# Kernel tuning notes

Hardware: AMD Instinct MI355X
Metric: run time of the kernel (lower is better)

Reference implementation:

```python
import jax, jax.numpy as jnp
import numpy as np

NUM_LAYERS = 4
EMBED = 1024
HEADS = 16
QKV = 1024
MLP = 4096
EPS_LN = 1e-6


def _layernorm(x, scale, bias):
    m = jnp.mean(x, axis=-1, keepdims=True)
    v = jnp.mean(jnp.square(x - m), axis=-1, keepdims=True)
    return (x - m) * jax.lax.rsqrt(v + EPS_LN) * scale + bias


def setup_inputs() -> dict:
    key = jax.random.key(0)
    ks = jax.random.split(key, 12)
    B, L = 4, 1024
    s = 0.02
    inp = {
        "queries": jax.random.normal(ks[0], (B, L, EMBED), dtype=jnp.float32),
        "Wq": jax.random.normal(ks[1], (NUM_LAYERS, EMBED, QKV), dtype=jnp.float32) * s,
        "bq": jnp.zeros((NUM_LAYERS, QKV), dtype=jnp.float32),
        "Wk": jax.random.normal(ks[2], (NUM_LAYERS, EMBED, QKV), dtype=jnp.float32) * s,
        "bk": jnp.zeros((NUM_LAYERS, QKV), dtype=jnp.float32),
        "Wv": jax.random.normal(ks[3], (NUM_LAYERS, EMBED, QKV), dtype=jnp.float32) * s,
        "bv": jnp.zeros((NUM_LAYERS, QKV), dtype=jnp.float32),
        "Wo": jax.random.normal(ks[4], (NUM_LAYERS, QKV, EMBED), dtype=jnp.float32) * s,
        "bo": jnp.zeros((NUM_LAYERS, EMBED), dtype=jnp.float32),
        "ln1_s": jnp.ones((NUM_LAYERS, EMBED), dtype=jnp.float32),
        "ln1_b": jnp.zeros((NUM_LAYERS, EMBED), dtype=jnp.float32),
        "ln2_s": jnp.ones((NUM_LAYERS, EMBED), dtype=jnp.float32),
        "ln2_b": jnp.zeros((NUM_LAYERS, EMBED), dtype=jnp.float32),
        "W1": jax.random.normal(ks[5], (NUM_LAYERS, EMBED, MLP), dtype=jnp.float32) * s,
        "b1": jnp.zeros((NUM_LAYERS, MLP), dtype=jnp.float32),
        "W2": jax.random.normal(ks[6], (NUM_LAYERS, MLP, EMBED), dtype=jnp.float32) * s,
        "b2": jnp.zeros((NUM_LAYERS, EMBED), dtype=jnp.float32),
    }
    return inp


def _block(x, Wq, bq, Wk, bk, Wv, bv, Wo, bo, ln1_s, ln1_b, ln2_s, ln2_b, W1, b1, W2, b2):
    # post-norm block (pre_norm=False)
    B, L, _ = x.shape
    head_dim = EMBED // HEADS
    q = (x @ Wq + bq).reshape(B, L, HEADS, head_dim)
    k = (x @ Wk + bk).reshape(B, L, HEADS, head_dim)
    v = (x @ Wv + bv).reshape(B, L, HEADS, head_dim)
    q = q / (head_dim ** 0.5)
    attn = jnp.einsum("bqhd,bkhd->bhqk", q, k)
    attn = jax.nn.softmax(attn, axis=-1)
    upd = jnp.einsum("bhqk,bkhd->bqhd", attn, v)  # [B,L,H,hd]
    a = upd.reshape(B, L, QKV) @ Wo + bo
    h = _layernorm(a + x, ln1_s, ln1_b)
    z = jax.nn.relu(h @ W1 + b1) @ W2 + b2
    return _layernorm(z + h, ln2_s, ln2_b)


def reference(queries, Wq, bq, Wk, bk, Wv, bv, Wo, bo, ln1_s, ln1_b, ln2_s, ln2_b, W1, b1, W2, b2):
    x = queries
    for l in range(NUM_LAYERS):
        x = _block(x, Wq[l], bq[l], Wk[l], bk[l], Wv[l], bv[l], Wo[l], bo[l],
                   ln1_s[l], ln1_b[l], ln2_s[l], ln2_b[l], W1[l], b1[l], W2[l], b2[l])
    return x
```

## Files before the change

kernel.cpp:

```cpp
#include <hip/hip_runtime.h>
#include <stdint.h>

typedef __bf16 bf16;
typedef __bf16 bf16x8 __attribute__((ext_vector_type(8)));
typedef float floatx4 __attribute__((ext_vector_type(4)));

#define LOG2E 1.44269504088896340736f

__device__ __forceinline__ void gl2lds16(const bf16* g, bf16* l) {
    __builtin_amdgcn_global_load_lds((__attribute__((address_space(1))) void*)g,
                                     (__attribute__((address_space(3))) void*)l,
                                     16, 0, 0);
}

template<int COLS>
__device__ __forceinline__ int swz(int ch, int r) {
    if constexpr (COLS == 32) return ch ^ ((r >> 1) & 3);
    else                      return ch ^ (r & 7);
}

template<int ROWS, int COLS>
__device__ __forceinline__ void stage_tile_sw(bf16* lds, const bf16* g, int srcStride, int wave, int lane) {
    constexpr int NINST = (ROWS * COLS * 2) / 1024;
    constexpr int ROWB  = COLS * 2;
    #pragma unroll
    for (int u = 0; u < NINST / 4; ++u) {
        int t  = wave + u * 4;
        int ob = t * 1024 + lane * 16;
        int r  = ob / ROWB;
        int ch = (ob % ROWB) >> 4;
        int sc = swz<COLS>(ch, r);
        gl2lds16(g + r * srcStride + sc * 8, lds + t * 512);
    }
}

template<int RELU, int OUTF, int OUTB>
__device__ __forceinline__ void gemm_core(const bf16* __restrict__ A, const bf16* __restrict__ Bt,
                                          const float* __restrict__ bias, float scale,
                                          float* __restrict__ outf, bf16* __restrict__ outb,
                                          int M, int N, int K, int m0, int n0) {
    __shared__ bf16 As[128 * 32];
    __shared__ bf16 Bs[128 * 32];
    const int tid = threadIdx.x, wave = tid >> 6, lane = tid & 63;
    const int wr = wave >> 1, wc = wave & 1;
    const int quad = lane >> 4, lq = lane & 15;
    const int swa = quad ^ ((lq >> 1) & 3);

    floatx4 acc[4][4] = {};
    const bf16* Ap = A + (size_t)m0 * K;
    const bf16* Bp = Bt + (size_t)n0 * K;

    for (int k0 = 0; k0 < K; k0 += 32) {
        stage_tile_sw<128, 32>(As, Ap + k0, K, wave, lane);
        stage_tile_sw<128, 32>(Bs, Bp + k0, K, wave, lane);
        __syncthreads();
        bf16x8 af[4], bfr[4];
        #pragma unroll
        for (int i = 0; i < 4; i++)
            af[i] = *(const bf16x8*)&As[(wr * 64 + i * 16 + lq) * 32 + swa * 8];
        #pragma unroll
        for (int j = 0; j < 4; j++)
            bfr[j] = *(const bf16x8*)&Bs[(wc * 64 + j * 16 + lq) * 32 + swa * 8];
        #pragma unroll
        for (int i = 0; i < 4; i++)
            #pragma unroll
            for (int j = 0; j < 4; j++)
                acc[i][j] = __builtin_amdgcn_mfma_f32_16x16x32_bf16(af[i], bfr[j], acc[i][j], 0, 0, 0);
        __syncthreads();
    }
    #pragma unroll
    for (int j = 0; j < 4; j++) {
        const int gc = n0 + wc * 64 + j * 16 + lq;
        const float bv = bias[gc];
        #pragma unroll
        for (int i = 0; i < 4; i++) {
            #pragma unroll
            for (int r = 0; r < 4; r++) {
                const int gr = m0 + wr * 64 + i * 16 + quad * 4 + r;
                float v = (acc[i][j][r] + bv) * scale;
                if (RELU) v = fmaxf(v, 0.f);
                if (OUTF) outf[(size_t)gr * N + gc] = v;
                if (OUTB) outb[(size_t)gr * N + gc] = (bf16)v;
            }
        }
    }
}

__global__ __launch_bounds__(256) void gemm_bf16relu(const bf16* A, const bf16* Bt, const float* bias,
                                                     bf16* out) {
    const int bid = blockIdx.x;
    const int xcd = bid & 7, j = bid >> 3;
    const int mt = xcd * 4 + (j >> 5);
    const int nt = j & 31;
    gemm_core<1, 0, 1>(A, Bt, bias, 1.f, nullptr, out, 4096, 4096, 1024, mt * 128, nt * 128);
}

__global__ __launch_bounds__(256) void gemm_qkv(const bf16* A, const bf16* Wt,
                                                const float* bq, const float* bk, const float* bv,
                                                bf16* out) {
    const int bid = blockIdx.x;
    const int xcd = bid & 7, j = bid >> 3;
    const int mloc = j / 24, r = j % 24;
    const int z = r >> 3, nt = r & 7;
    const int mt = xcd * 4 + mloc;
    const bf16* Bt = Wt + (size_t)z * 1024 * 1024;
    const float* bias = (z == 0) ? bq : (z == 1) ? bk : bv;
    bf16* o = out + (size_t)z * 4096 * 1024;
    const float scale = (z == 0) ? 0.125f * LOG2E : 1.f;
    gemm_core<0, 0, 1>(A, Bt, bias, scale, nullptr, o, 4096, 1024, 1024, mt * 128, nt * 128);
}

__global__ __launch_bounds__(256) void gemm_n1024(const bf16* __restrict__ A, const bf16* __restrict__ Bt,
                                                  const float* __restrict__ bias, float* __restrict__ out,
                                                  int K) {
    __shared__ bf16 As[128 * 64];
    __shared__ bf16 Bs[64 * 64];
    const int bid = blockIdx.x;
    const int xcd = bid & 7, j = bid >> 3;
    const int sk = j >> 6, j2 = j & 63;
    const int mt = xcd * 4 + (j2 >> 4);
    const int nt = j2 & 15;
    const int m0 = mt * 128, n0 = nt * 64;
    const int Kh = K >> 1;
    const int tid = threadIdx.x, wave = tid >> 6, lane = tid & 63;
    const int wr = wave >> 1, wc = wave & 1;
    const int quad = lane >> 4, lq = lane & 15;

    floatx4 acc[4][2] = {};
    const bf16* Ap = A + (size_t)m0 * K + (size_t)sk * Kh;
    const bf16* Bp = Bt + (size_t)n0 * K + (size_t)sk * Kh;

    for (int k0 = 0; k0 < Kh; k0 += 64) {
        stage_tile_sw<128, 64>(As, Ap + k0, K, wave, lane);
        stage_tile_sw<64, 64>(Bs, Bp + k0, K, wave, lane);
        __syncthreads();
        #pragma unroll
        for (int kk = 0; kk < 2; kk++) {
            const int chs = ((kk * 4 + quad) ^ (lq & 7)) * 8;
            bf16x8 af[4], bfr[2];
            #pragma unroll
            for (int i = 0; i < 4; i++)
                af[i] = *(const bf16x8*)&As[(wr * 64 + i * 16 + lq) * 64 + chs];
            #pragma unroll
            for (int jj = 0; jj < 2; jj++)
                bfr[jj] = *(const bf16x8*)&Bs[(wc * 32 + jj * 16 + lq) * 64 + chs];
            #pragma unroll
            for (int i = 0; i < 4; i++)
                #pragma unroll
                for (int jj = 0; jj < 2; jj++)
                    acc[i][jj] = __builtin_amdgcn_mfma_f32_16x16x32_bf16(af[i], bfr[jj], acc[i][jj], 0, 0, 0);
        }
        __syncthreads();
    }
    float* op = out + (size_t)sk * 4194304;
    #pragma unroll
    for (int jj = 0; jj < 2; jj++) {
        const int gc = n0 + wc * 32 + jj * 16 + lq;
        const float bv = sk ? 0.f : bias[gc];
        #pragma unroll
        for (int i = 0; i < 4; i++)
            #pragma unroll
            for (int r = 0; r < 4; r++) {
                const int gr = m0 + wr * 64 + i * 16 + quad * 4 + r;
                op[(size_t)gr * 1024 + gc] = acc[i][jj][r] + bv;
            }
    }
}

__device__ __forceinline__ void ttile(const float* __restrict__ src, bf16* __restrict__ dst,
                                      int K, int N, int n0, int k0) {
    __shared__ float t[32][33];
    const int tx = threadIdx.x & 31, ty = threadIdx.x >> 5;
    #pragma unroll
    for (int i = 0; i < 4; i++)
        t[ty + i * 8][tx] = src[(size_t)(k0 + ty + i * 8) * N + n0 + tx];
    __syncthreads();
    #pragma unroll
    for (int i = 0; i < 4; i++)
        dst[(size_t)(n0 + ty + i * 8) * K + k0 + tx] = (bf16)t[tx][ty + i * 8];
}

__global__ __launch_bounds__(256) void transpose_all(const float* Wq, const float* Wk, const float* Wv,
                                                     const float* Wo, const float* W1, const float* W2,
                                                     bf16* qkvT, bf16* oT, bf16* w1T, bf16* w2T) {
    const int bx = blockIdx.x;
    if (bx < 4096) {
        const int z = bx >> 10, tile = bx & 1023;
        const float* s = (z == 0) ? Wq : (z == 1) ? Wk : (z == 2) ? Wv : Wo;
        bf16* d = (z == 3) ? oT : qkvT + (size_t)z * 1048576;
        ttile(s, d, 1024, 1024, (tile & 31) * 32, (tile >> 5) * 32);
    } else if (bx < 8192) {
        const int tile = bx - 4096;
        ttile(W1, w1T, 1024, 4096, (tile & 127) * 32, (tile >> 7) * 32);
    } else {
        const int tile = bx - 8192;
        ttile(W2, w2T, 4096, 1024, (tile & 31) * 32, (tile >> 5) * 32);
    }
}

__global__ __launch_bounds__(256) void transpose_v(const bf16* v, bf16* vT) {
    __shared__ float t[128][34];
    const int l0 = blockIdx.x * 128, d0 = blockIdx.y * 32, bh = blockIdx.z;
    const int b = bh >> 4, h = bh & 15;
    const int tid = threadIdx.x;
    const int dp = (tid & 15) * 2, lr = tid >> 4;
    #pragma unroll
    for (int i = 0; i < 8; i++) {
        const int lrow = lr + i * 16;
        bf16 two[2];
        *(uint32_t*)two = *(const uint32_t*)&v[(size_t)(b * 1024 + l0 + lrow) * 1024 + h * 64 + d0 + dp];
        t[lrow][dp]     = (float)two[0];
        t[lrow][dp + 1] = (float)two[1];
    }
    __syncthreads();
    #pragma unroll
    for (int u2 = 0; u2 < 2; u2++) {
        const int c = tid + u2 * 256;
        const int d = c >> 4, lp = c & 15;
        bf16 pb[8];
        #pragma unroll
        for (int j = 0; j < 8; j++)
            pb[j] = (bf16)t[j * 16 + lp][d];
        *(bf16x8*)&vT[((size_t)bh * 64 + d0 + d) * 1024 + l0 + lp * 8] = *(bf16x8*)pb;
    }
}

__global__ __launch_bounds__(256) void cvt_f32_bf16(const float* src, bf16* dst) {
    const int i = (blockIdx.x * 256 + threadIdx.x) * 4;
    const float4 v = *(const float4*)(src + i);
    bf16 t4[4] = {(bf16)v.x, (bf16)v.y, (bf16)v.z, (bf16)v.w};
    *(uint64_t*)(dst + i) = *(const uint64_t*)t4;
}

__global__ __launch_bounds__(256) void ln_kernel(const float* __restrict__ a, const float* __restrict__ a2,
                                                 const float* __restrict__ res,
                                                 const float* __restrict__ gamma, const float* __restrict__ beta,
                                                 float* __restrict__ outf, bf16* __restrict__ outb) {
    const int row = blockIdx.x, tid = threadIdx.x;
    const size_t base = (size_t)row * 1024 + tid * 4;
    const float4 av  = *(const float4*)(a + base);
    const float4 a2v = *(const float4*)(a2 + base);
    const float4 rv  = *(const float4*)(res + base);
    float x0 = av.x + a2v.x + rv.x, x1 = av.y + a2v.y + rv.y;
    float x2 = av.z + a2v.z + rv.z, x3 = av.w + a2v.w + rv.w;
    float s  = x0 + x1 + x2 + x3;
    float sq = x0 * x0 + x1 * x1 + x2 * x2 + x3 * x3;
    #pragma unroll
    for (int off = 32; off; off >>= 1) {
        s  += __shfl_xor(s,  off, 64);
        sq += __shfl_xor(sq, off, 64);
    }
    __shared__ float red[8];
    const int wave = tid >> 6, lane = tid & 63;
    if (lane == 0) { red[wave] = s; red[wave + 4] = sq; }
    __syncthreads();
    const float S  = red[0] + red[1] + red[2] + red[3];
    const float SQ = red[4] + red[5] + red[6] + red[7];
    const float mean = S * (1.f / 1024.f);
    const float var  = SQ * (1.f / 1024.f) - mean * mean;
    const float rstd = rsqrtf(var + 1e-6f);
    const int c = tid * 4;
    const float4 g  = *(const float4*)(gamma + c);
    const float4 be = *(const float4*)(beta + c);
    float y0 = (x0 - mean) * rstd * g.x + be.x;
    float y1 = (x1 - mean) * rstd * g.y + be.y;
    float y2 = (x2 - mean) * rstd * g.z + be.z;
    float y3 = (x3 - mean) * rstd * g.w + be.w;
    float4 yo; yo.x = y0; yo.y = y1; yo.z = y2; yo.w = y3;
    *(float4*)(outf + base) = yo;
    bf16 t4[4] = {(bf16)y0, (bf16)y1, (bf16)y2, (bf16)y3};
    *(uint64_t*)(outb + base) = *(const uint64_t*)t4;
}

__global__ __launch_bounds__(256, 2) void attn_kernel(const bf16* __restrict__ Q, const bf16* __restrict__ Kg,
                                                      const bf16* __restrict__ Vt, bf16* __restrict__ O) {
    __shared__ bf16 Ks[128 * 64];
    __shared__ bf16 Vs[64 * 128];
    __shared__ bf16 Ps[128 * 128];
    const int bh = blockIdx.x, qt = blockIdx.y;
    const int b = bh >> 4, h = bh & 15;
    const int tid = threadIdx.x, wave = tid >> 6, lane = tid & 63;
    const int quad = lane >> 4, lq = lane & 15;

    const bf16* qg = Q + ((size_t)b * 1024 + qt * 128) * 1024 + h * 64;
    const bf16* kg = Kg + (size_t)b * 1024 * 1024 + h * 64;
    const bf16* vg = Vt + (size_t)bh * 64 * 1024;

    stage_tile_sw<128, 64>(Ps, qg, 1024, wave, lane);
    __syncthreads();
    bf16x8 aq[2][2];
    #pragma unroll
    for (int i = 0; i < 2; i++)
        #pragma unroll
        for (int kk = 0; kk < 2; kk++) {
            const int row = wave * 32 + i * 16 + lq;
            const int chs = (kk * 4 + quad) ^ (lq & 7);
            aq[i][kk] = *(const bf16x8*)&Ps[row * 64 + chs * 8];
        }

    floatx4 oacc[2][4] = {};
    float lsum[2][4] = {};

    for (int kt = 0; kt < 1024; kt += 128) {
        stage_tile_sw<128, 64>(Ks, kg + (size_t)kt * 1024, 1024, wave, lane);
        stage_tile_sw<64, 128>(Vs, vg + kt, 1024, wave, lane);
        __syncthreads();

        floatx4 sacc[2][8] = {};
        #pragma unroll
        for (int kk = 0; kk < 2; kk++)
            #pragma unroll
            for (int j = 0; j < 8; j++) {
                const int chs = (kk * 4 + quad) ^ (lq & 7);
                bf16x8 bk = *(const bf16x8*)&Ks[(j * 16 + lq) * 64 + chs * 8];
                sacc[0][j] = __builtin_amdgcn_mfma_f32_16x16x32_bf16(aq[0][kk], bk, sacc[0][j], 0, 0, 0);
                sacc[1][j] = __builtin_amdgcn_mfma_f32_16x16x32_bf16(aq[1][kk], bk, sacc[1][j], 0, 0, 0);
            }

        #pragma unroll
        for (int i = 0; i < 2; i++)
            #pragma unroll
            for (int r = 0; r < 4; r++) {
                const int row = wave * 32 + i * 16 + quad * 4 + r;
                float ls = 0.f;
                bf16 pb[8];
                #pragma unroll
                for (int j = 0; j < 8; j++) {
                    const float pv = exp2f(sacc[i][j][r]);
                    ls += pv;
                    pb[j] = (bf16)pv;
                }
                lsum[i][r] += ls;
                *(bf16x8*)&Ps[row * 128 + (lq ^ (row & 7)) * 8] = *(const bf16x8*)pb;
            }

        #pragma unroll
        for (int kk = 0; kk < 4; kk++) {
            bf16x8 ap[2];
            #pragma unroll
            for (int i = 0; i < 2; i++) {
                const int row = wave * 32 + i * 16 + lq;
                const int chs = (kk * 4 + quad) ^ (lq & 7);
                ap[i] = *(const bf16x8*)&Ps[row * 128 + chs * 8];
            }
            #pragma unroll
            for (int dj = 0; dj < 4; dj++) {
                const int chs = (kk * 4 + quad) ^ (lq & 7);
                bf16x8 bv = *(const bf16x8*)&Vs[(dj * 16 + lq) * 128 + chs * 8];
                oacc[0][dj] = __builtin_amdgcn_mfma_f32_16x16x32_bf16(ap[0], bv, oacc[0][dj], 0, 0, 0);
                oacc[1][dj] = __builtin_amdgcn_mfma_f32_16x16x32_bf16(ap[1], bv, oacc[1][dj], 0, 0, 0);
            }
        }
        __syncthreads();
    }

    #pragma unroll
    for (int i = 0; i < 2; i++)
        #pragma unroll
        for (int r = 0; r < 4; r++) {
            float l = lsum[i][r];
            l += __shfl_xor(l, 1, 64); l += __shfl_xor(l, 2, 64);
            l += __shfl_xor(l, 4, 64); l += __shfl_xor(l, 8, 64);
            lsum[i][r] = 1.f / l;
        }
    #pragma unroll
    for (int i = 0; i < 2; i++)
        #pragma unroll
        for (int dj = 0; dj < 4; dj++)
            #pragma unroll
            for (int r = 0; r < 4; r++) {
                const int row = qt * 128 + wave * 32 + i * 16 + quad * 4 + r;
                O[((size_t)b * 1024 + row) * 1024 + h * 64 + dj * 16 + lq] = (bf16)(oacc[i][dj][r] * lsum[i][r]);
            }
}

extern "C" void kernel_launch(void* const* d_in, const int* in_sizes, int n_in,
                              void* d_out, int out_size, void* d_ws, size_t ws_size,
                              hipStream_t stream) {
    const float* queries = (const float*)d_in[0];
    const float* Wq = (const float*)d_in[1];  const float* bq = (const float*)d_in[2];
    const float* Wk = (const float*)d_in[3];  const float* bk = (const float*)d_in[4];
    const float* Wv = (const float*)d_in[5];  const float* bv = (const float*)d_in[6];
    const float* Wo = (const float*)d_in[7];  const float* bo = (const float*)d_in[8];
    const float* ln1_s = (const float*)d_in[9];   const float* ln1_b = (const float*)d_in[10];
    const float* ln2_s = (const float*)d_in[11];  const float* ln2_b = (const float*)d_in[12];
    const float* W1 = (const float*)d_in[13]; const float* b1 = (const float*)d_in[14];
    const float* W2 = (const float*)d_in[15]; const float* b2 = (const float*)d_in[16];

    char* p = (char*)d_ws;
    size_t off = 0;
    auto take = [&](size_t bytes) { void* r = p + off; off += bytes; return r; };
    bf16*  WqkvT = (bf16*)take(6291456);
    bf16*  WoT   = (bf16*)take(2097152);
    bf16*  W1T   = (bf16*)take(8388608);
    bf16*  W2T   = (bf16*)take(8388608);
    bf16*  x_bf  = (bf16*)take(8388608);
    float* xf    = (float*)take(16777216);
    bf16*  qkvb  = (bf16*)take(25165824);
    bf16*  vTb   = (bf16*)take(8388608);
    bf16*  updb  = (bf16*)take(8388608);
    float* az    = (float*)take(33554432);
    float* hf    = (float*)take(16777216);
    bf16*  hbf   = (bf16*)take(8388608);
    bf16*  tmlp  = (bf16*)take(33554432);

    cvt_f32_bf16<<<4096, 256, 0, stream>>>(queries, x_bf);

    for (int l = 0; l < 4; ++l) {
        const size_t w1k = (size_t)l * 1024 * 1024;
        const size_t w4m = (size_t)l * 4096 * 1024;
        transpose_all<<<12288, 256, 0, stream>>>(Wq + w1k, Wk + w1k, Wv + w1k, Wo + w1k,
                                                 W1 + w4m, W2 + w4m, WqkvT, WoT, W1T, W2T);

        gemm_qkv<<<768, 256, 0, stream>>>(x_bf, WqkvT,
                                          bq + l * 1024, bk + l * 1024, bv + l * 1024, qkvb);
        transpose_v<<<dim3(8, 2, 64), 256, 0, stream>>>(qkvb + 2 * 4194304, vTb);
        attn_kernel<<<dim3(64, 8), 256, 0, stream>>>(qkvb, qkvb + 4194304, vTb, updb);
        gemm_n1024<<<1024, 256, 0, stream>>>(updb, WoT, bo + l * 1024, az, 1024);
        ln_kernel<<<4096, 256, 0, stream>>>(az, az + 4194304, (l == 0) ? queries : xf,
                                            ln1_s + l * 1024, ln1_b + l * 1024, hf, hbf);
        gemm_bf16relu<<<1024, 256, 0, stream>>>(hbf, W1T, b1 + l * 4096, tmlp);
        gemm_n1024<<<1024, 256, 0, stream>>>(tmlp, W2T, b2 + l * 1024, az, 4096);
        ln_kernel<<<4096, 256, 0, stream>>>(az, az + 4194304, hf, ln2_s + l * 1024, ln2_b + l * 1024,
                                            (l == 3) ? (float*)d_out : xf, x_bf);
    }
}
```

Baseline: 1.089 ms.

## Replace MLP1 GEMM with 256x256-tile, 8-wave double-buffered pipelined kernel

Swaps the 128x128-tile, 4-wave MLP up-projection GEMM for a new kernel with 256x256 output tiles, 512 threads, BK=64 and double-buffered LDS. Loads for the next K tile are interleaved with the MFMA work, and wave priority is raised around the MFMA bursts. The goal is more operand reuse per byte loaded and global-load latency hidden behind compute. The larger tile cuts the grid to 256 blocks and uses about 128KB of LDS per block, which may lower occupancy and raise tail effects on 256 CUs.

```diff
diff --git a/kernel.cpp b/kernel.cpp
--- a/kernel.cpp
+++ b/kernel.cpp
@@ -30,6 +30,18 @@
         int r  = ob / ROWB;
         int ch = (ob % ROWB) >> 4;
         int sc = swz<COLS>(ch, r);
+        gl2lds16(g + r * srcStride + sc * 8, lds + t * 512);
+    }
+}
+
+__device__ __forceinline__ void stage_half_512(bf16* lds, const bf16* g, int srcStride, int wave, int lane) {
+    #pragma unroll
+    for (int u = 0; u < 2; ++u) {
+        int t  = wave + u * 8;
+        int ob = t * 1024 + lane * 16;
+        int r  = ob >> 7;
+        int ch = (ob >> 4) & 7;
+        int sc = ch ^ (r & 7);
         gl2lds16(g + r * srcStride + sc * 8, lds + t * 512);
     }
 }
@@ -86,13 +98,92 @@
     }
 }
 
-__global__ __launch_bounds__(256) void gemm_bf16relu(const bf16* A, const bf16* Bt, const float* bias,
-                                                     bf16* out) {
+__global__ __launch_bounds__(512, 2) void gemm_mlp1(const bf16* __restrict__ A, const bf16* __restrict__ Bt,
+                                                    const float* __restrict__ bias, bf16* __restrict__ out) {
+    __shared__ bf16 As[2][2][128 * 64];
+    __shared__ bf16 Bs[2][2][128 * 64];
     const int bid = blockIdx.x;
     const int xcd = bid & 7, j = bid >> 3;
-    const int mt = xcd * 4 + (j >> 5);
-    const int nt = j & 31;
-    gemm_core<1, 0, 1>(A, Bt, bias, 1.f, nullptr, out, 4096, 4096, 1024, mt * 128, nt * 128);
+    const int mt = xcd * 2 + (j >> 4), nt = j & 15;
+    const int m0 = mt * 256, n0 = nt * 256;
+    const int tid = threadIdx.x, wave = tid >> 6, lane = tid & 63;
+    const int wr = wave >> 2;
+    const int wcn = wave & 3;
+    const int bwh = wcn >> 1, bwl = wcn & 1;
+    const int quad = lane >> 4, lq = lane & 15;
+    constexpr int K = 1024;
+
+    const bf16* Ab0 = A + (size_t)m0 * K;
+    const bf16* Ab1 = A + (size_t)(m0 + 128) * K;
+    const bf16* Bb0 = Bt + (size_t)n0 * K;
+    const bf16* Bb1 = Bt + (size_t)(n0 + 128) * K;
+
+    floatx4 acc[8][4] = {};
+
+    stage_half_512(As[0][0], Ab0, K, wave, lane);
+    stage_half_512(As[0][1], Ab1, K, wave, lane);
+    stage_half_512(Bs[0][0], Bb0, K, wave, lane);
+    stage_half_512(Bs[0][1], Bb1, K, wave, lane);
+
+    for (int kt = 0; kt < 16; ++kt) {
+        const int cur = kt & 1, nxt = cur ^ 1;
+        const int k1 = (kt + 1) * 64;
+        const bool pf = (kt < 15);
+        __syncthreads();
+        const bf16* Ar = As[cur][wr];
+        const bf16* Br = Bs[cur][bwh];
+        #pragma unroll
+        for (int mh = 0; mh < 2; mh++) {
+            bf16x8 af[4][2];
+            if (mh == 0 && pf) stage_half_512(As[nxt][0], Ab0 + k1, K, wave, lane);
+            #pragma unroll
+            for (int i2 = 0; i2 < 4; i2++)
+                #pragma unroll
+                for (int kk = 0; kk < 2; kk++)
+                    af[i2][kk] = *(const bf16x8*)&Ar[(mh * 64 + i2 * 16 + lq) * 64 +
+                                                     (((kk * 4 + quad) ^ (lq & 7)) * 8)];
+            if (pf) {
+                if (mh == 0) stage_half_512(As[nxt][1], Ab1 + k1, K, wave, lane);
+                else         stage_half_512(Bs[nxt][1], Bb1 + k1, K, wave, lane);
+            }
+            #pragma unroll
+            for (int nh = 0; nh < 2; nh++) {
+                bf16x8 bfr[2][2];
+                #pragma unroll
+                for (int j2 = 0; j2 < 2; j2++)
+                    #pragma unroll
+                    for (int kk = 0; kk < 2; kk++)
+                        bfr[j2][kk] = *(const bf16x8*)&Br[(bwl * 64 + nh * 32 + j2 * 16 + lq) * 64 +
+                                                          (((kk * 4 + quad) ^ (lq & 7)) * 8)];
+                if (mh == 0 && nh == 1 && pf) stage_half_512(Bs[nxt][0], Bb0 + k1, K, wave, lane);
+                __builtin_amdgcn_s_setprio(1);
+                #pragma unroll
+                for (int i2 = 0; i2 < 4; i2++)
+                    #pragma unroll
+                    for (int j2 = 0; j2 < 2; j2++)
+                        #pragma unroll
+                        for (int kk = 0; kk < 2; kk++)
+                            acc[mh * 4 + i2][nh * 2 + j2] =
+                                __builtin_amdgcn_mfma_f32_16x16x32_bf16(af[i2][kk], bfr[j2][kk],
+                                                                        acc[mh * 4 + i2][nh * 2 + j2], 0, 0, 0);
+                __builtin_amdgcn_s_setprio(0);
+            }
+        }
+    }
+
+    #pragma unroll
+    for (int j2 = 0; j2 < 4; j2++) {
+        const int gc = n0 + bwh * 128 + bwl * 64 + j2 * 16 + lq;
+        const float bv = bias[gc];
+        #pragma unroll
+        for (int i2 = 0; i2 < 8; i2++)
+            #pragma unroll
+            for (int r = 0; r < 4; r++) {
+                const int gr = m0 + wr * 128 + i2 * 16 + quad * 4 + r;
+                float v = acc[i2][j2][r] + bv;
+                out[(size_t)gr * 4096 + gc] = (bf16)fmaxf(v, 0.f);
+            }
+    }
 }
 
 __global__ __launch_bounds__(256) void gemm_qkv(const bf16* A, const bf16* Wt,
@@ -419,7 +510,7 @@
         gemm_n1024<<<1024, 256, 0, stream>>>(updb, WoT, bo + l * 1024, az, 1024);
         ln_kernel<<<4096, 256, 0, stream>>>(az, az + 4194304, (l == 0) ? queries : xf,
                                             ln1_s + l * 1024, ln1_b + l * 1024, hf, hbf);
-        gemm_bf16relu<<<1024, 256, 0, stream>>>(hbf, W1T, b1 + l * 4096, tmlp);
+        gemm_mlp1<<<256, 512, 0, stream>>>(hbf, W1T, b1 + l * 4096, tmlp);
         gemm_n1024<<<1024, 256, 0, stream>>>(tmlp, W2T, b2 + l * 1024, az, 4096);
         ln_kernel<<<4096, 256, 0, stream>>>(az, az + 4194304, hf, ln2_s + l * 1024, ln2_b + l * 1024,
                                             (l == 3) ? (float*)d_out : xf, x_bf);
```

New measurement: 1.034 ms. -5.1%, faster.
